# Kernel tuning notes

Measured on AMD Instinct MI355X. Metric: run time of the kernel, lower is better.

Reference implementation:

```python
import jax, jax.numpy as jnp
import numpy as np

B, C = 1, 1
D = H = W = 128          # volume depth/height/width (z, y, x)
V = U = 128              # detector rows (v) / cols (u)
A = 96                   # projection angles
N_STEPS = 128            # Joseph ray-marching steps
SX = SY = SD = 1.0       # voxel size (sd, sy, sx)
SU = SV = 1.0            # detector spacing (sv, su)


def setup_inputs() -> dict:
    key = jax.random.key(0)
    # model-facing volume [B, C, X, Y, Z]
    vol = jax.random.normal(key, (B, C, W, H, D), dtype=jnp.float32)
    angles = jnp.linspace(0.0, np.pi, A, endpoint=False).astype(jnp.float32)
    return {"vol": vol, "angles": angles}


def _corner(idx, size):
    """Floor/ceil corner indices + zero-padded linear weights (align_corners=True,
    padding_mode='zeros' semantics of F.grid_sample)."""
    i0f = jnp.floor(idx)
    frac = idx - i0f
    i0 = i0f.astype(jnp.int32)
    i1 = i0 + 1
    w0 = jnp.where((i0 >= 0) & (i0 < size), 1.0 - frac, 0.0)
    w1 = jnp.where((i1 >= 0) & (i1 < size), frac, 0.0)
    return jnp.clip(i0, 0, size - 1), jnp.clip(i1, 0, size - 1), w0, w1


def reference(vol, angles):
    # [B,C,X,Y,Z] -> [B,C,D,H,W] (z,y,x ordering used internally)
    v_zyx = jnp.transpose(vol, (0, 1, 4, 3, 2))
    cos_t = jnp.cos(angles)[:, None]   # [A,1]
    sin_t = jnp.sin(angles)[:, None]   # [A,1]
    u = (jnp.arange(U, dtype=jnp.float32) - (U - 1) / 2.0) * SU   # [U]
    v = (jnp.arange(V, dtype=jnp.float32) - (V - 1) / 2.0) * SV   # [V]
    # half ray length = half in-plane diagonal
    T = 0.5 * float(np.sqrt(((W - 1) * SX) ** 2 + ((H - 1) * SY) ** 2))
    delta_t = 2.0 * T / float(N_STEPS)

    x_base = -u[None, :] * sin_t   # [A,U] ray point at t=0
    y_base = u[None, :] * cos_t    # [A,U]
    # z depends only on detector row v; constant along the ray
    z_idx = v / SD + (D - 1) / 2.0                     # [V]
    z0, z1, wz0, wz1 = _corner(z_idx, D)
    z0, z1 = z0[:, None], z1[:, None]                  # [V,1]
    wz0, wz1 = wz0[:, None], wz1[:, None]

    t_vals = -T + (jnp.arange(N_STEPS, dtype=jnp.float32) + 0.5) * delta_t

    def step(acc, t):
        x_idx = (x_base + t * cos_t) / SX + (W - 1) / 2.0   # [A,U]
        y_idx = (y_base + t * sin_t) / SY + (H - 1) / 2.0   # [A,U]
        x0, x1, wx0, wx1 = [a[:, None, :] for a in _corner(x_idx, W)]  # [A,1,U]
        y0, y1, wy0, wy1 = [a[:, None, :] for a in _corner(y_idx, H)]  # [A,1,U]
        g = lambda zi, yi, xi: v_zyx[:, :, zi, yi, xi]      # -> [B,C,A,V,U]
        s = (wz0 * (wy0 * (wx0 * g(z0, y0, x0) + wx1 * g(z0, y0, x1))
                    + wy1 * (wx0 * g(z0, y1, x0) + wx1 * g(z0, y1, x1)))
             + wz1 * (wy0 * (wx0 * g(z1, y0, x0) + wx1 * g(z1, y0, x1))
                      + wy1 * (wx0 * g(z1, y1, x0) + wx1 * g(z1, y1, x1))))
        return acc + s, None

    acc0 = jnp.zeros((B, C, A, V, U), dtype=vol.dtype)
    acc, _ = jax.lax.scan(jax.checkpoint(step), acc0, t_vals)
    sino = acc * jnp.float32(delta_t)            # [B,C,A,V,U]
    # model-facing sinogram [B,C,X=U,A,Z=V]
    return jnp.transpose(sino, (0, 1, 4, 2, 3))
```

## Files before the change

kernel.cpp:

```cpp
#include <hip/hip_runtime.h>
#include <hip/hip_fp16.h>

namespace {
constexpr int A_N = 96;
constexpr int U_N = 128;
constexpr int V_N = 128;
constexpr int W_N = 128;
constexpr int H_N = 128;
constexpr int NSTEPS = 128;
constexpr float T_HALF = 89.80256121069154f;
constexpr float DT = 1.4031650189170554f;
constexpr float INV_DT = 1.0f / DT;
constexpr int PAD = 6;
constexpr int WP = W_N + 2 * PAD;
constexpr int ROW_BYTES = WP * 256;
constexpr int RAYS_PER_BLOCK = 8;
constexpr int BLOCK_THREADS = RAYS_PER_BLOCK * 16;
constexpr int SEGS = 2;
constexpr size_t VOLP_COLS = (size_t)WP * WP;
constexpr size_t VOLP_BYTES = VOLP_COLS * 256;
constexpr size_t SINO = (size_t)U_N * A_N * V_N;
}

__device__ __forceinline__ unsigned int packh2(float a, float b) {
    return (unsigned int)__half_as_ushort(__float2half_rn(a)) |
           ((unsigned int)__half_as_ushort(__float2half_rn(b)) << 16);
}

__global__ __launch_bounds__(256) void vol_pad_f16(
    const float* __restrict__ vol, unsigned int* __restrict__ volp)
{
    const int idx = blockIdx.x * 256 + threadIdx.x;
    if (idx >= (int)(VOLP_COLS * 16)) return;
    const int zo  = idx & 15;
    const int col = idx >> 4;
    const int yp = col % WP;
    const int xp = col / WP;
    const int x = xp - PAD;
    const int y = yp - PAD;
    uint4 o = make_uint4(0u, 0u, 0u, 0u);
    if ((unsigned)x < 128u && (unsigned)y < 128u) {
        const float* src = vol + (((size_t)x * 128 + y) << 7) + zo * 8;
        const float4 f0 = *(const float4*)(src);
        const float4 f1 = *(const float4*)(src + 4);
        o.x = packh2(f0.x, f0.y);
        o.y = packh2(f0.z, f0.w);
        o.z = packh2(f1.x, f1.y);
        o.w = packh2(f1.z, f1.w);
    }
    *(uint4*)((char*)volp + (size_t)col * 256 + zo * 16) = o;
}

__device__ __forceinline__ const char* step_base(
    const char* volc, int lane16, float i_f, float cv, float sv, float xb, float yb,
    float& fx, float& fy)
{
    const float tf = fmaf(i_f + 0.5f, DT, -T_HALF);
    const float xi = fmaf(tf, cv, xb);
    const float yi = fmaf(tf, sv, yb);
    const float fx0 = floorf(xi);
    const float fy0 = floorf(yi);
    fx = xi - fx0;
    fy = yi - fy0;
    const int x0 = (int)fx0;
    const int y0 = (int)fy0;
    const int base = (((x0 + PAD) * WP + (y0 + PAD)) << 8) + lane16;
    return volc + base;
}

__device__ __forceinline__ void consume(
    const uint4& q00, const uint4& q01, const uint4& q10, const uint4& q11,
    float fx, float fy, float* accf)
{
    const float wx0 = 1.f - fx;
    const float wy0 = 1.f - fy;
    const __half2 w00 = __float2half2_rn(wx0 * wy0);
    const __half2 w01 = __float2half2_rn(wx0 * fy);
    const __half2 w10 = __float2half2_rn(fx  * wy0);
    const __half2 w11 = __float2half2_rn(fx  * fy);
    const __half2* h00 = (const __half2*)&q00;
    const __half2* h01 = (const __half2*)&q01;
    const __half2* h10 = (const __half2*)&q10;
    const __half2* h11 = (const __half2*)&q11;
#pragma unroll
    for (int j = 0; j < 4; ++j) {
        __half2 p = __hmul2(w00, h00[j]);
        p = __hfma2(w01, h01[j], p);
        p = __hfma2(w10, h10[j], p);
        p = __hfma2(w11, h11[j], p);
        const float2 f = __half22float2(p);
        accf[2 * j]     += f.x;
        accf[2 * j + 1] += f.y;
    }
}

__global__ __launch_bounds__(BLOCK_THREADS) void joseph_fwd_inc(
    const unsigned short* __restrict__ volp,
    const float* __restrict__ angles,
    float* __restrict__ dst, float scale)
{
    const int zo  = threadIdx.x & 15;
    const int r   = threadIdx.x >> 4;
    const int u_i = blockIdx.x * RAYS_PER_BLOCK + r;
    const int a   = blockIdx.y;

    const int spseg = NSTEPS / gridDim.z;
    const int i0 = blockIdx.z * spseg;
    const int i1 = i0 + spseg;

    const float ang = angles[a];
    const float cv = cosf(ang);
    const float sv = sinf(ang);
    const float up = (float)u_i - 63.5f;
    const float xb = fmaf(-up, sv, 63.5f);
    const float yb = fmaf( up, cv, 63.5f);

    float tlo = -2.f * T_HALF, thi = 2.f * T_HALF;
    if (fabsf(cv) > 1e-6f) {
        const float ta = (-1.f - xb) / cv, tb = (128.f - xb) / cv;
        tlo = fmaxf(tlo, fminf(ta, tb));
        thi = fminf(thi, fmaxf(ta, tb));
    } else if (xb <= -1.f || xb >= 128.f) { thi = tlo - 1.f; }
    if (fabsf(sv) > 1e-6f) {
        const float ta = (-1.f - yb) / sv, tb = (128.f - yb) / sv;
        tlo = fmaxf(tlo, fminf(ta, tb));
        thi = fminf(thi, fmaxf(ta, tb));
    } else if (yb <= -1.f || yb >= 128.f) { thi = tlo - 1.f; }
    const int ilo = (int)floorf(fmaf(tlo + T_HALF, INV_DT, -0.5f)) - 1;
    const int ihi = (int)ceilf (fmaf(thi + T_HALF, INV_DT, -0.5f)) + 1;
    int lo = min(max(ilo, i0), i1);
    int hi = min(max(ihi + 1, i0), i1);
    lo &= ~1;
    hi = (hi + 1) & ~1;

    const char* __restrict__ volc = (const char*)volp;
    const int lane16 = zo << 4;

    float accf[8];
#pragma unroll
    for (int k = 0; k < 8; ++k) accf[k] = 0.f;

    for (int i = lo; i < hi; i += 2) {
        float fxA, fyA, fxB, fyB;
        const char* pA = step_base(volc, lane16, (float)i,       cv, sv, xb, yb, fxA, fyA);
        const char* pB = step_base(volc, lane16, (float)(i + 1), cv, sv, xb, yb, fxB, fyB);

        const uint4 qA00 = *(const uint4*)(pA);
        const uint4 qA01 = *(const uint4*)(pA + 256);
        const uint4 qA10 = *(const uint4*)(pA + ROW_BYTES);
        const uint4 qA11 = *(const uint4*)(pA + ROW_BYTES + 256);
        const uint4 qB00 = *(const uint4*)(pB);
        const uint4 qB01 = *(const uint4*)(pB + 256);
        const uint4 qB10 = *(const uint4*)(pB + ROW_BYTES);
        const uint4 qB11 = *(const uint4*)(pB + ROW_BYTES + 256);

        consume(qA00, qA01, qA10, qA11, fxA, fyA, accf);
        consume(qB00, qB01, qB10, qB11, fxB, fyB, accf);
    }

    float* op = dst + (size_t)blockIdx.z * SINO + ((size_t)u_i * A_N + a) * V_N + 8 * zo;
    *(float4*)(op)     = make_float4(accf[0] * scale, accf[1] * scale, accf[2] * scale, accf[3] * scale);
    *(float4*)(op + 4) = make_float4(accf[4] * scale, accf[5] * scale, accf[6] * scale, accf[7] * scale);
}

__global__ __launch_bounds__(256) void reduce_segs2(
    const float4* __restrict__ p, float4* __restrict__ out)
{
    const size_t i = (size_t)blockIdx.x * 256 + threadIdx.x;
    const size_t q = SINO / 4;
    const float4 a = p[i];
    const float4 b = p[i + q];
    out[i] = make_float4((a.x + b.x) * DT, (a.y + b.y) * DT,
                         (a.z + b.z) * DT, (a.w + b.w) * DT);
}

__global__ __launch_bounds__(256) void joseph_fwd_f32(
    const float* __restrict__ vol,
    const float* __restrict__ angles,
    float* __restrict__ out)
{
    const int zo  = threadIdx.x & 15;
    const int r   = threadIdx.x >> 4;
    const int u_i = blockIdx.x * 16 + r;
    const int a   = blockIdx.y;

    const float ang = angles[a];
    const float c = cosf(ang);
    const float s = sinf(ang);
    const float u = (float)u_i - 63.5f;
    const float xb = fmaf(-u, s, 63.5f);
    const float yb = fmaf( u, c, 63.5f);

    const float* volz = vol + 8 * zo;
    float4 accA = make_float4(0.f, 0.f, 0.f, 0.f);
    float4 accB = make_float4(0.f, 0.f, 0.f, 0.f);

    for (int i = 0; i < NSTEPS; ++i) {
        const float t  = fmaf((float)i + 0.5f, DT, -T_HALF);
        const float xi = fmaf(t, c, xb);
        const float yi = fmaf(t, s, yb);
        const float fx0f = floorf(xi);
        const float fy0f = floorf(yi);
        const int x0 = (int)fx0f;
        const int y0 = (int)fy0f;
        const float fx = xi - fx0f;
        const float fy = yi - fy0f;
        const int x1 = x0 + 1;
        const int y1 = y0 + 1;
        const float wx0 = (x0 >= 0 && x0 < W_N) ? (1.f - fx) : 0.f;
        const float wx1 = (x1 >= 0 && x1 < W_N) ? fx : 0.f;
        const float wy0 = (y0 >= 0 && y0 < H_N) ? (1.f - fy) : 0.f;
        const float wy1 = (y1 >= 0 && y1 < H_N) ? fy : 0.f;
        if ((wx0 + wx1) == 0.f || (wy0 + wy1) == 0.f) continue;
        const int cx0 = min(max(x0, 0), W_N - 1);
        const int cx1 = min(max(x1, 0), W_N - 1);
        const int cy0 = min(max(y0, 0), H_N - 1);
        const int cy1 = min(max(y1, 0), H_N - 1);
        const float* p00 = volz + ((cx0 * H_N + cy0) << 7);
        const float* p01 = volz + ((cx1 * H_N + cy0) << 7);
        const float* p10 = volz + ((cx0 * H_N + cy1) << 7);
        const float* p11 = volz + ((cx1 * H_N + cy1) << 7);
        const float4 v00a = *(const float4*)(p00);
        const float4 v00b = *(const float4*)(p00 + 4);
        const float4 v01a = *(const float4*)(p01);
        const float4 v01b = *(const float4*)(p01 + 4);
        const float4 v10a = *(const float4*)(p10);
        const float4 v10b = *(const float4*)(p10 + 4);
        const float4 v11a = *(const float4*)(p11);
        const float4 v11b = *(const float4*)(p11 + 4);
        const float w00 = wx0 * wy0, w01 = wx1 * wy0, w10 = wx0 * wy1, w11 = wx1 * wy1;
        accA.x = fmaf(w00, v00a.x, fmaf(w01, v01a.x, fmaf(w10, v10a.x, fmaf(w11, v11a.x, accA.x))));
        accA.y = fmaf(w00, v00a.y, fmaf(w01, v01a.y, fmaf(w10, v10a.y, fmaf(w11, v11a.y, accA.y))));
        accA.z = fmaf(w00, v00a.z, fmaf(w01, v01a.z, fmaf(w10, v10a.z, fmaf(w11, v11a.z, accA.z))));
        accA.w = fmaf(w00, v00a.w, fmaf(w01, v01a.w, fmaf(w10, v10a.w, fmaf(w11, v11a.w, accA.w))));
        accB.x = fmaf(w00, v00b.x, fmaf(w01, v01b.x, fmaf(w10, v10b.x, fmaf(w11, v11b.x, accB.x))));
        accB.y = fmaf(w00, v00b.y, fmaf(w01, v01b.y, fmaf(w10, v10b.y, fmaf(w11, v11b.y, accB.y))));
        accB.z = fmaf(w00, v00b.z, fmaf(w01, v01b.z, fmaf(w10, v10b.z, fmaf(w11, v11b.z, accB.z))));
        accB.w = fmaf(w00, v00b.w, fmaf(w01, v01b.w, fmaf(w10, v10b.w, fmaf(w11, v11b.w, accB.w))));
    }

    float* op = out + ((size_t)u_i * A_N + a) * V_N + 8 * zo;
    *(float4*)(op)     = make_float4(accA.x * DT, accA.y * DT, accA.z * DT, accA.w * DT);
    *(float4*)(op + 4) = make_float4(accB.x * DT, accB.y * DT, accB.z * DT, accB.w * DT);
}

extern "C" void kernel_launch(void* const* d_in, const int* in_sizes, int n_in,
                              void* d_out, int out_size, void* d_ws, size_t ws_size,
                              hipStream_t stream) {
    const float* vol    = (const float*)d_in[0];
    const float* angles = (const float*)d_in[1];
    float* out          = (float*)d_out;

    const size_t need_full = VOLP_BYTES + SEGS * SINO * sizeof(float);
    const int pad_blocks = (int)((VOLP_COLS * 16 + 255) / 256);

    if (ws_size >= VOLP_BYTES) {
        unsigned int* volp = (unsigned int*)d_ws;
        hipLaunchKernelGGL(vol_pad_f16, dim3(pad_blocks), dim3(256), 0, stream, vol, volp);
        if (ws_size >= need_full) {
            float* partial = (float*)((char*)d_ws + VOLP_BYTES);
            dim3 grid(U_N / RAYS_PER_BLOCK, A_N, SEGS);
            hipLaunchKernelGGL(joseph_fwd_inc, grid, dim3(BLOCK_THREADS), 0, stream,
                               (const unsigned short*)volp, angles, partial, 1.0f);
            hipLaunchKernelGGL(reduce_segs2, dim3(SINO / 4 / 256), dim3(256), 0, stream,
                               (const float4*)partial, (float4*)out);
        } else {
            dim3 grid(U_N / RAYS_PER_BLOCK, A_N, 1);
            hipLaunchKernelGGL(joseph_fwd_inc, grid, dim3(BLOCK_THREADS), 0, stream,
                               (const unsigned short*)volp, angles, out, DT);
        }
    } else {
        dim3 grid(U_N / 16, A_N);
        hipLaunchKernelGGL(joseph_fwd_f32, grid, dim3(256), 0, stream, vol, angles, out);
    }
}
```

Measured before the change: 111.3 us.

## Widen per-thread z work, accumulate in half2, reorder blocks, add 4-way step split

Each thread now handles 16 z values (8 threads per ray, 16 rays per block) and issues 32-byte loads per corner. The bilinear sum now builds up in half2 registers and is flushed to fp32 every four steps, replacing the per-step conversion and fp32 adds. Blocks along u are issued centre-out, so the longer rays near the volume centre start first. The step range can split into 4 segments when workspace allows, with a generic reduce kernel. This trades more fp16 accumulation error, more registers per thread and more partial-sum memory traffic for fewer conversions and more parallelism.

```diff
diff --git a/kernel.cpp b/kernel.cpp
--- a/kernel.cpp
+++ b/kernel.cpp
@@ -14,9 +14,9 @@
 constexpr int PAD = 6;
 constexpr int WP = W_N + 2 * PAD;
 constexpr int ROW_BYTES = WP * 256;
-constexpr int RAYS_PER_BLOCK = 8;
-constexpr int BLOCK_THREADS = RAYS_PER_BLOCK * 16;
-constexpr int SEGS = 2;
+constexpr int ZT = 8;
+constexpr int RAYS_PER_BLOCK = 16;
+constexpr int BLOCK_THREADS = RAYS_PER_BLOCK * ZT;
 constexpr size_t VOLP_COLS = (size_t)WP * WP;
 constexpr size_t VOLP_BYTES = VOLP_COLS * 256;
 constexpr size_t SINO = (size_t)U_N * A_N * V_N;
@@ -52,7 +52,7 @@
 }
 
 __device__ __forceinline__ const char* step_base(
-    const char* volc, int lane16, float i_f, float cv, float sv, float xb, float yb,
+    const char* volc, int laneb, float i_f, float cv, float sv, float xb, float yb,
     float& fx, float& fy)
 {
     const float tf = fmaf(i_f + 0.5f, DT, -T_HALF);
@@ -64,13 +64,12 @@
     fy = yi - fy0;
     const int x0 = (int)fx0;
     const int y0 = (int)fy0;
-    const int base = (((x0 + PAD) * WP + (y0 + PAD)) << 8) + lane16;
+    const int base = (((x0 + PAD) * WP + (y0 + PAD)) << 8) + laneb;
     return volc + base;
 }
 
-__device__ __forceinline__ void consume(
-    const uint4& q00, const uint4& q01, const uint4& q10, const uint4& q11,
-    float fx, float fy, float* accf)
+__device__ __forceinline__ void consume16(
+    const uint4* q, float fx, float fy, __half2* hacc)
 {
     const float wx0 = 1.f - fx;
     const float wy0 = 1.f - fy;
@@ -78,30 +77,29 @@
     const __half2 w01 = __float2half2_rn(wx0 * fy);
     const __half2 w10 = __float2half2_rn(fx  * wy0);
     const __half2 w11 = __float2half2_rn(fx  * fy);
-    const __half2* h00 = (const __half2*)&q00;
-    const __half2* h01 = (const __half2*)&q01;
-    const __half2* h10 = (const __half2*)&q10;
-    const __half2* h11 = (const __half2*)&q11;
-#pragma unroll
-    for (int j = 0; j < 4; ++j) {
-        __half2 p = __hmul2(w00, h00[j]);
-        p = __hfma2(w01, h01[j], p);
-        p = __hfma2(w10, h10[j], p);
-        p = __hfma2(w11, h11[j], p);
-        const float2 f = __half22float2(p);
-        accf[2 * j]     += f.x;
-        accf[2 * j + 1] += f.y;
-    }
-}
-
-__global__ __launch_bounds__(BLOCK_THREADS) void joseph_fwd_inc(
+    const __half2* h00 = (const __half2*)&q[0];
+    const __half2* h01 = (const __half2*)&q[2];
+    const __half2* h10 = (const __half2*)&q[4];
+    const __half2* h11 = (const __half2*)&q[6];
+#pragma unroll
+    for (int j = 0; j < 8; ++j) {
+        hacc[j] = __hfma2(w00, h00[j], hacc[j]);
+        hacc[j] = __hfma2(w01, h01[j], hacc[j]);
+        hacc[j] = __hfma2(w10, h10[j], hacc[j]);
+        hacc[j] = __hfma2(w11, h11[j], hacc[j]);
+    }
+}
+
+__global__ __launch_bounds__(BLOCK_THREADS, 4) void joseph_fwd_inc(
     const unsigned short* __restrict__ volp,
     const float* __restrict__ angles,
     float* __restrict__ dst, float scale)
 {
-    const int zo  = threadIdx.x & 15;
-    const int r   = threadIdx.x >> 4;
-    const int u_i = blockIdx.x * RAYS_PER_BLOCK + r;
+    const int zo = threadIdx.x & (ZT - 1);
+    const int r  = threadIdx.x >> 3;
+    const int bx = (int)blockIdx.x;
+    const int xt = (bx & 1) ? (4 + (bx >> 1)) : (3 - (bx >> 1));
+    const int u_i = xt * RAYS_PER_BLOCK + r;
     const int a   = blockIdx.y;
 
     const int spseg = NSTEPS / gridDim.z;
@@ -134,44 +132,77 @@
     hi = (hi + 1) & ~1;
 
     const char* __restrict__ volc = (const char*)volp;
-    const int lane16 = zo << 4;
-
-    float accf[8];
-#pragma unroll
-    for (int k = 0; k < 8; ++k) accf[k] = 0.f;
-
+    const int laneb = zo << 5;
+
+    __half2 hacc[8];
+    float accf[16];
+#pragma unroll
+    for (int j = 0; j < 8; ++j) hacc[j] = __float2half2_rn(0.f);
+#pragma unroll
+    for (int k = 0; k < 16; ++k) accf[k] = 0.f;
+
+    int kc = 0;
     for (int i = lo; i < hi; i += 2) {
         float fxA, fyA, fxB, fyB;
-        const char* pA = step_base(volc, lane16, (float)i,       cv, sv, xb, yb, fxA, fyA);
-        const char* pB = step_base(volc, lane16, (float)(i + 1), cv, sv, xb, yb, fxB, fyB);
-
-        const uint4 qA00 = *(const uint4*)(pA);
-        const uint4 qA01 = *(const uint4*)(pA + 256);
-        const uint4 qA10 = *(const uint4*)(pA + ROW_BYTES);
-        const uint4 qA11 = *(const uint4*)(pA + ROW_BYTES + 256);
-        const uint4 qB00 = *(const uint4*)(pB);
-        const uint4 qB01 = *(const uint4*)(pB + 256);
-        const uint4 qB10 = *(const uint4*)(pB + ROW_BYTES);
-        const uint4 qB11 = *(const uint4*)(pB + ROW_BYTES + 256);
-
-        consume(qA00, qA01, qA10, qA11, fxA, fyA, accf);
-        consume(qB00, qB01, qB10, qB11, fxB, fyB, accf);
-    }
-
-    float* op = dst + (size_t)blockIdx.z * SINO + ((size_t)u_i * A_N + a) * V_N + 8 * zo;
-    *(float4*)(op)     = make_float4(accf[0] * scale, accf[1] * scale, accf[2] * scale, accf[3] * scale);
-    *(float4*)(op + 4) = make_float4(accf[4] * scale, accf[5] * scale, accf[6] * scale, accf[7] * scale);
-}
-
-__global__ __launch_bounds__(256) void reduce_segs2(
-    const float4* __restrict__ p, float4* __restrict__ out)
+        const char* pA = step_base(volc, laneb, (float)i,       cv, sv, xb, yb, fxA, fyA);
+        const char* pB = step_base(volc, laneb, (float)(i + 1), cv, sv, xb, yb, fxB, fyB);
+
+        uint4 qA[8], qB[8];
+        qA[0] = *(const uint4*)(pA);
+        qA[1] = *(const uint4*)(pA + 16);
+        qA[2] = *(const uint4*)(pA + 256);
+        qA[3] = *(const uint4*)(pA + 272);
+        qA[4] = *(const uint4*)(pA + ROW_BYTES);
+        qA[5] = *(const uint4*)(pA + ROW_BYTES + 16);
+        qA[6] = *(const uint4*)(pA + ROW_BYTES + 256);
+        qA[7] = *(const uint4*)(pA + ROW_BYTES + 272);
+        qB[0] = *(const uint4*)(pB);
+        qB[1] = *(const uint4*)(pB + 16);
+        qB[2] = *(const uint4*)(pB + 256);
+        qB[3] = *(const uint4*)(pB + 272);
+        qB[4] = *(const uint4*)(pB + ROW_BYTES);
+        qB[5] = *(const uint4*)(pB + ROW_BYTES + 16);
+        qB[6] = *(const uint4*)(pB + ROW_BYTES + 256);
+        qB[7] = *(const uint4*)(pB + ROW_BYTES + 272);
+
+        consume16(qA, fxA, fyA, hacc);
+        consume16(qB, fxB, fyB, hacc);
+
+        if (((++kc) & 1) == 0) {
+#pragma unroll
+            for (int j = 0; j < 8; ++j) {
+                const float2 f = __half22float2(hacc[j]);
+                accf[2 * j]     += f.x;
+                accf[2 * j + 1] += f.y;
+                hacc[j] = __float2half2_rn(0.f);
+            }
+        }
+    }
+#pragma unroll
+    for (int j = 0; j < 8; ++j) {
+        const float2 f = __half22float2(hacc[j]);
+        accf[2 * j]     += f.x;
+        accf[2 * j + 1] += f.y;
+    }
+
+    float* op = dst + (size_t)blockIdx.z * SINO + ((size_t)u_i * A_N + a) * V_N + 16 * zo;
+    *(float4*)(op)      = make_float4(accf[0]  * scale, accf[1]  * scale, accf[2]  * scale, accf[3]  * scale);
+    *(float4*)(op + 4)  = make_float4(accf[4]  * scale, accf[5]  * scale, accf[6]  * scale, accf[7]  * scale);
+    *(float4*)(op + 8)  = make_float4(accf[8]  * scale, accf[9]  * scale, accf[10] * scale, accf[11] * scale);
+    *(float4*)(op + 12) = make_float4(accf[12] * scale, accf[13] * scale, accf[14] * scale, accf[15] * scale);
+}
+
+__global__ __launch_bounds__(256) void reduce_segs(
+    const float4* __restrict__ p, float4* __restrict__ out, int nseg)
 {
     const size_t i = (size_t)blockIdx.x * 256 + threadIdx.x;
     const size_t q = SINO / 4;
-    const float4 a = p[i];
-    const float4 b = p[i + q];
-    out[i] = make_float4((a.x + b.x) * DT, (a.y + b.y) * DT,
-                         (a.z + b.z) * DT, (a.w + b.w) * DT);
+    float4 s = p[i];
+    for (int k = 1; k < nseg; ++k) {
+        const float4 b = p[i + (size_t)k * q];
+        s.x += b.x; s.y += b.y; s.z += b.z; s.w += b.w;
+    }
+    out[i] = make_float4(s.x * DT, s.y * DT, s.z * DT, s.w * DT);
 }
 
 __global__ __launch_bounds__(256) void joseph_fwd_f32(
@@ -251,19 +282,23 @@
     const float* angles = (const float*)d_in[1];
     float* out          = (float*)d_out;
 
-    const size_t need_full = VOLP_BYTES + SEGS * SINO * sizeof(float);
     const int pad_blocks = (int)((VOLP_COLS * 16 + 255) / 256);
 
     if (ws_size >= VOLP_BYTES) {
         unsigned int* volp = (unsigned int*)d_ws;
         hipLaunchKernelGGL(vol_pad_f16, dim3(pad_blocks), dim3(256), 0, stream, vol, volp);
-        if (ws_size >= need_full) {
+
+        int nseg = 0;
+        if (ws_size >= VOLP_BYTES + 4 * SINO * sizeof(float))      nseg = 4;
+        else if (ws_size >= VOLP_BYTES + 2 * SINO * sizeof(float)) nseg = 2;
+
+        if (nseg) {
             float* partial = (float*)((char*)d_ws + VOLP_BYTES);
-            dim3 grid(U_N / RAYS_PER_BLOCK, A_N, SEGS);
+            dim3 grid(U_N / RAYS_PER_BLOCK, A_N, nseg);
             hipLaunchKernelGGL(joseph_fwd_inc, grid, dim3(BLOCK_THREADS), 0, stream,
                                (const unsigned short*)volp, angles, partial, 1.0f);
-            hipLaunchKernelGGL(reduce_segs2, dim3(SINO / 4 / 256), dim3(256), 0, stream,
-                               (const float4*)partial, (float4*)out);
+            hipLaunchKernelGGL(reduce_segs, dim3(SINO / 4 / 256), dim3(256), 0, stream,
+                               (const float4*)partial, (float4*)out, nseg);
         } else {
             dim3 grid(U_N / RAYS_PER_BLOCK, A_N, 1);
             hipLaunchKernelGGL(joseph_fwd_inc, grid, dim3(BLOCK_THREADS), 0, stream,
```

Measured after the change: 121.7 us. 9.3% more time.
